# Kernel tuning notes

Measured on AMD Instinct MI355X. Metric: run time of the kernel, lower is better.

The kernel has to match this reference:

```python
import jax, jax.numpy as jnp
import numpy as np

B, N, C = 8, 16384, 256
HEADS = 8
TOK = 4  # token_size = (4, 4)


def _unfold3(x):
    # x: (b, c, h, w) -> (b, c, 9, h, w); 3x3 neighborhood, zero padded.
    b, c, h, w = x.shape
    p = jnp.pad(x, ((0, 0), (0, 0), (1, 1), (1, 1)))
    pat = jnp.stack([p[:, :, 1 + dy:1 + dy + h, 1 + dx:1 + dx + w]
                     for dy in (-1, 0, 1) for dx in (-1, 0, 1)], axis=2)
    return pat


def _fold3(u):
    # u: (b, k, 9, h, w) -> (b, k, h, w); scatter-add inverse of _unfold3
    # (matches F.conv_transpose2d with eye(9) kernels, stride 1, pad 1).
    b, k, _, h, w = u.shape
    p = jnp.pad(u, ((0, 0), (0, 0), (0, 0), (1, 1), (1, 1)))
    out = jnp.zeros((b, k, h, w), u.dtype)
    i = 0
    for dy in (-1, 0, 1):
        for dx in (-1, 0, 1):
            out = out + p[:, :, i, 1 - dy:1 - dy + h, 1 - dx:1 - dx + w]
            i += 1
    return out


def setup_inputs() -> dict:
    key = jax.random.key(0)
    k1, k2, k3, k4 = jax.random.split(key, 4)
    x = jax.random.normal(k1, (B, N, C), jnp.float32)
    qkv_w = jax.random.normal(k2, (3 * C, C), jnp.float32) * 0.02
    proj_w = jax.random.normal(k3, (C, C), jnp.float32) * 0.02
    proj_b = jax.random.normal(k4, (C,), jnp.float32) * 0.02
    return {"x": x, "qkv_w": qkv_w, "proj_w": proj_w, "proj_b": proj_b}


def reference(x, qkv_w, proj_w, proj_b):
    b, n, c = x.shape
    H = W = int(np.sqrt(n))
    hh, ww = H // TOK, W // TOK
    nw = hh * ww                      # number of super tokens
    scale = c ** -0.5
    hd = c // HEADS
    head_scale = hd ** -0.5

    xi = jnp.transpose(x, (0, 2, 1)).reshape(b, c, H, W)
    blocks = xi.reshape(b, c, hh, TOK, ww, TOK)
    wf = blocks.mean(axis=(3, 5))                      # (b,c,hh,ww) adaptive avg pool
    pix = blocks.transpose(0, 2, 4, 3, 5, 1).reshape(b, nw, TOK * TOK, c)

    # 3x3 super-token neighborhood features: (b, nw, c, 9)
    wfu = _unfold3(wf).reshape(b, c, 9, nw).transpose(0, 3, 1, 2)

    # pixel <-> super-token affinity, softmax over 9 neighbors
    aff = jax.nn.softmax(jnp.einsum('bnpc,bnck->bnpk', pix, wfu) * scale, axis=-1)

    # normalization: fold of per-window affinity mass -> (b,1,hh,ww)
    aff_sum = _fold3(aff.sum(2).transpose(0, 2, 1).reshape(b, 1, 9, hh, ww))

    # aggregate pixels into super tokens and fold neighborhoods back
    wf2 = jnp.einsum('bnpc,bnpk->bnck', pix, aff)      # (b,nw,c,9)
    wf2 = _fold3(wf2.transpose(0, 2, 3, 1).reshape(b, c, 9, hh, ww))  # (b,c,hh,ww)
    wf2 = wf2 / (jax.lax.stop_gradient(aff_sum) + 1e-12)

    # inner attention over super tokens (non-SDPA: softmax over key axis)
    qkv = jnp.einsum('oc,bchw->bohw', qkv_w, wf2).reshape(b, HEADS, 3 * hd, nw)
    q, k, v = jnp.split(qkv, 3, axis=2)                # each (b,heads,hd,nw)
    attn = jnp.einsum('bhdn,bhdm->bhnm', k, q) * head_scale
    attn = jax.nn.softmax(attn, axis=-2)               # softmax over key index n
    ref = jnp.einsum('bhdn,bhnm->bhdm', v, attn).reshape(b, c, hh, ww)
    ref = jnp.einsum('oc,bchw->bohw', proj_w, ref) + proj_b[None, :, None, None]

    # scatter refined super tokens back to pixels through the affinity
    wfu2 = _unfold3(ref).reshape(b, c, 9, nw).transpose(0, 3, 1, 2)   # (b,nw,c,9)
    pix2 = jnp.einsum('bnck,bnpk->bncp', wfu2, aff)    # (b,nw,c,16)
    pix2 = pix2.reshape(b, hh, ww, c, TOK, TOK).transpose(0, 3, 1, 4, 2, 5)
    pix2 = pix2.reshape(b, c, H, W)
    # NOTE: torch does a raw memory reshape (B,C,H,W)->(B,H*W,C), not a transpose;
    # we replicate that exactly.
    return pix2.reshape(b, H * W, c)
```

## Files before the change

### kernel.cpp

```cpp
#include <hip/hip_runtime.h>

typedef short short8 __attribute__((ext_vector_type(8)));
typedef float f32x4 __attribute__((ext_vector_type(4)));

__device__ __forceinline__ unsigned short f2bf(float x) {
  union { float f; unsigned int u; } v; v.f = x;
  unsigned int r = (v.u + 0x7FFFu + ((v.u >> 16) & 1u)) >> 16;
  return (unsigned short)r;
}

__global__ __launch_bounds__(256) void k0_wconv(const float* __restrict__ qkvw,
                                                const float* __restrict__ projw,
                                                unsigned short* __restrict__ wqkvbf,
                                                unsigned short* __restrict__ wprojbf) {
  int i = blockIdx.x * 256 + threadIdx.x;
  if (i < 768 * 256) wqkvbf[i] = f2bf(qkvw[i]);
  if (i < 256 * 256) wprojbf[i] = f2bf(projw[i]);
}

__global__ __launch_bounds__(256) void k1_pool(const float* __restrict__ x,
                                               float* __restrict__ wf) {
  int t = threadIdx.x;
  int blk = blockIdx.x;
  int b = blk >> 10, pos = blk & 1023;
  int y = pos >> 5, xw = pos & 31;
  const float* xb = x + (size_t)b * 4194304;
  float acc = 0.f;
  #pragma unroll
  for (int p = 0; p < 16; ++p) {
    int h = 4 * y + (p >> 2), w = 4 * xw + (p & 3);
    acc += xb[(size_t)(h * 128 + w) * 256 + t];
  }
  wf[(size_t)blk * 256 + t] = acc * 0.0625f;
}

__global__ __launch_bounds__(256) void k2_winaff(const float* __restrict__ x,
                                                 const float* __restrict__ wf,
                                                 float* __restrict__ aff_g,
                                                 float* __restrict__ wf2acc,
                                                 float* __restrict__ asumacc) {
  __shared__ float pixs[16][257];
  __shared__ float wfu[9][257];
  __shared__ float aff_s[16][12];
  int t = threadIdx.x;
  int blk = blockIdx.x;
  int b = blk >> 10, pos = blk & 1023;
  int y = pos >> 5, xw = pos & 31;
  const float* xb = x + (size_t)b * 4194304;

  #pragma unroll
  for (int p = 0; p < 16; ++p) {
    int h = 4 * y + (p >> 2), w = 4 * xw + (p & 3);
    pixs[p][t] = xb[(size_t)(h * 128 + w) * 256 + t];
  }
  #pragma unroll
  for (int i = 0; i < 9; ++i) {
    int dy = i / 3 - 1, dx = i % 3 - 1;
    int ny = y + dy, nx = xw + dx;
    float v = 0.f;
    if (ny >= 0 && ny < 32 && nx >= 0 && nx < 32)
      v = wf[((size_t)(b * 1024) + ny * 32 + nx) * 256 + t];
    wfu[i][t] = v;
  }
  __syncthreads();

  if (t < 144) {
    int p = t / 9, i = t - p * 9;
    float acc = 0.f;
    #pragma unroll 8
    for (int c = 0; c < 256; ++c) acc += pixs[p][c] * wfu[i][c];
    aff_s[p][i] = acc * 0.0625f;
  }
  __syncthreads();

  if (t < 16) {
    float m = aff_s[t][0];
    #pragma unroll
    for (int i = 1; i < 9; ++i) m = fmaxf(m, aff_s[t][i]);
    float e[9]; float s = 0.f;
    #pragma unroll
    for (int i = 0; i < 9; ++i) { e[i] = __expf(aff_s[t][i] - m); s += e[i]; }
    float inv = 1.f / s;
    #pragma unroll
    for (int i = 0; i < 9; ++i) aff_s[t][i] = e[i] * inv;
  }
  __syncthreads();

  if (t < 144) aff_g[(size_t)blk * 144 + t] = aff_s[t / 9][t % 9];

  if (t < 9) {
    int dy = t / 3 - 1, dx = t % 3 - 1;
    int ny = y + dy, nx = xw + dx;
    if (ny >= 0 && ny < 32 && nx >= 0 && nx < 32) {
      float s = 0.f;
      #pragma unroll
      for (int p = 0; p < 16; ++p) s += aff_s[p][t];
      atomicAdd(&asumacc[b * 1024 + ny * 32 + nx], s);
    }
  }

  #pragma unroll
  for (int i = 0; i < 9; ++i) {
    int dy = i / 3 - 1, dx = i % 3 - 1;
    int ny = y + dy, nx = xw + dx;
    if (ny < 0 || ny >= 32 || nx < 0 || nx >= 32) continue;
    float acc = 0.f;
    #pragma unroll
    for (int p = 0; p < 16; ++p) acc += pixs[p][t] * aff_s[p][i];
    atomicAdd(&wf2acc[((size_t)(b * 1024) + ny * 32 + nx) * 256 + t], acc);
  }
}

__global__ __launch_bounds__(256) void k3_norm(const float* __restrict__ wf2acc,
                                               const float* __restrict__ asumacc,
                                               unsigned short* __restrict__ wf2bf) {
  int t = threadIdx.x;
  for (int u = blockIdx.x; u < 8192; u += 2048) {
    float den = asumacc[u] + 1e-12f;
    float v = wf2acc[(size_t)u * 256 + t] / den;
    wf2bf[(size_t)u * 256 + t] = f2bf(v);
  }
}

__global__ __launch_bounds__(256) void k4_qkv(const unsigned short* __restrict__ wbf,
                                              const unsigned short* __restrict__ xbf,
                                              unsigned short* __restrict__ qt,
                                              unsigned short* __restrict__ kt,
                                              unsigned short* __restrict__ vt) {
  int tid = threadIdx.x, lane = tid & 63, wv = tid >> 6;
  int l15 = lane & 15, g = lane >> 4;
  int nb = blockIdx.x * 64 + (wv & 1) * 32;
  int ob = blockIdx.y * 64 + (wv >> 1) * 32;
  int b = blockIdx.z;
  const unsigned short* X = xbf + (size_t)b * 262144;
  f32x4 acc[2][2] = {};
  for (int cc = 0; cc < 256; cc += 32) {
    short8 af[2], bfr[2];
    #pragma unroll
    for (int oi = 0; oi < 2; ++oi)
      af[oi] = *(const short8*)(wbf + (size_t)(ob + oi * 16 + l15) * 256 + cc + g * 8);
    #pragma unroll
    for (int ni = 0; ni < 2; ++ni)
      bfr[ni] = *(const short8*)(X + (size_t)(nb + ni * 16 + l15) * 256 + cc + g * 8);
    #pragma unroll
    for (int oi = 0; oi < 2; ++oi)
      #pragma unroll
      for (int ni = 0; ni < 2; ++ni)
        acc[oi][ni] = __builtin_amdgcn_mfma_f32_16x16x32_bf16(af[oi], bfr[ni], acc[oi][ni], 0, 0, 0);
  }
  #pragma unroll
  for (int oi = 0; oi < 2; ++oi)
    #pragma unroll
    for (int ni = 0; ni < 2; ++ni)
      #pragma unroll
      for (int r = 0; r < 4; ++r) {
        int o = ob + oi * 16 + g * 4 + r;
        int n = nb + ni * 16 + l15;
        unsigned short bv = f2bf(acc[oi][ni][r]);
        int head = o / 96;
        int rr = o - head * 96;
        size_t bh = (size_t)(b * 8 + head);
        if (rr < 32) qt[(bh * 1024 + n) * 32 + rr] = bv;
        else if (rr < 64) kt[(bh * 1024 + n) * 32 + (rr - 32)] = bv;
        else vt[(bh * 32 + (rr - 64)) * 1024 + n] = bv;
      }
}

__global__ __launch_bounds__(256) void k5_attn(const unsigned short* __restrict__ qt,
                                               const unsigned short* __restrict__ kt,
                                               const unsigned short* __restrict__ vt,
                                               unsigned short* __restrict__ refpre) {
  __shared__ short P_lds[4][32][40];
  __shared__ float out_lds[4][32][33];
  __shared__ float den_lds[4][32];
  int tid = threadIdx.x, lane = tid & 63, wv = tid >> 6;
  int l15 = lane & 15, g = lane >> 4;
  int mt = blockIdx.x, h = blockIdx.y, b = blockIdx.z;
  const unsigned short* qtb = qt + ((size_t)(b * 8 + h) * 1024) * 32;
  const unsigned short* ktb = kt + ((size_t)(b * 8 + h) * 1024) * 32;
  const unsigned short* vtb = vt + ((size_t)(b * 8 + h) * 32) * 1024;

  short8 qf[2];
  #pragma unroll
  for (int mi = 0; mi < 2; ++mi) {
    int m = mt * 32 + mi * 16 + l15;
    qf[mi] = *(const short8*)(qtb + (size_t)m * 32 + g * 8);
  }
  f32x4 oacc[2][2] = {};
  float dsum0 = 0.f, dsum1 = 0.f;
  const float hs = 0.17677669529663687f;

  for (int c8 = 0; c8 < 8; ++c8) {
    int nchunk = wv * 256 + c8 * 32;
    f32x4 sf[2][2];
    #pragma unroll
    for (int nt = 0; nt < 2; ++nt) {
      int n = nchunk + nt * 16 + l15;
      short8 kf = *(const short8*)(ktb + (size_t)n * 32 + g * 8);
      #pragma unroll
      for (int mi = 0; mi < 2; ++mi) {
        f32x4 z = {0.f, 0.f, 0.f, 0.f};
        sf[nt][mi] = __builtin_amdgcn_mfma_f32_16x16x32_bf16(kf, qf[mi], z, 0, 0, 0);
      }
    }
    #pragma unroll
    for (int nt = 0; nt < 2; ++nt)
      #pragma unroll
      for (int mi = 0; mi < 2; ++mi) {
        float p0 = __expf(hs * sf[nt][mi][0]);
        float p1 = __expf(hs * sf[nt][mi][1]);
        float p2 = __expf(hs * sf[nt][mi][2]);
        float p3 = __expf(hs * sf[nt][mi][3]);
        float ds = (p0 + p1) + (p2 + p3);
        if (mi == 0) dsum0 += ds; else dsum1 += ds;
        unsigned int w01 = ((unsigned int)f2bf(p1) << 16) | f2bf(p0);
        unsigned int w23 = ((unsigned int)f2bf(p3) << 16) | f2bf(p2);
        int ml = mi * 16 + l15;
        int nn = nt * 16 + g * 4;
        *(unsigned int*)&P_lds[wv][ml][nn] = w01;
        *(unsigned int*)&P_lds[wv][ml][nn + 2] = w23;
      }
    #pragma unroll
    for (int dh = 0; dh < 2; ++dh) {
      short8 vf = *(const short8*)(vtb + (size_t)(dh * 16 + l15) * 1024 + nchunk + g * 8);
      #pragma unroll
      for (int mi = 0; mi < 2; ++mi) {
        short8 pf = *(const short8*)&P_lds[wv][mi * 16 + l15][g * 8];
        oacc[dh][mi] = __builtin_amdgcn_mfma_f32_16x16x32_bf16(vf, pf, oacc[dh][mi], 0, 0, 0);
      }
    }
  }

  dsum0 += __shfl_xor(dsum0, 16); dsum0 += __shfl_xor(dsum0, 32);
  dsum1 += __shfl_xor(dsum1, 16); dsum1 += __shfl_xor(dsum1, 32);
  if (lane < 16) { den_lds[wv][lane] = dsum0; den_lds[wv][16 + lane] = dsum1; }
  #pragma unroll
  for (int dh = 0; dh < 2; ++dh)
    #pragma unroll
    for (int mi = 0; mi < 2; ++mi)
      #pragma unroll
      for (int r = 0; r < 4; ++r)
        out_lds[wv][dh * 16 + g * 4 + r][mi * 16 + l15] = oacc[dh][mi][r];
  __syncthreads();

  #pragma unroll
  for (int kk = 0; kk < 4; ++kk) {
    int idx = kk * 256 + tid;
    int d = idx & 31, m = idx >> 5;
    float v = out_lds[0][d][m] + out_lds[1][d][m] + out_lds[2][d][m] + out_lds[3][d][m];
    float den = den_lds[0][m] + den_lds[1][m] + den_lds[2][m] + den_lds[3][m];
    float res = v / den;
    int n = mt * 32 + m;
    refpre[((size_t)(b * 1024) + n) * 256 + h * 32 + d] = f2bf(res);
  }
}

__global__ __launch_bounds__(256) void k6_proj(const unsigned short* __restrict__ wbf,
                                               const unsigned short* __restrict__ xbf,
                                               const float* __restrict__ bias,
                                               float* __restrict__ reft) {
  int tid = threadIdx.x, lane = tid & 63, wv = tid >> 6;
  int l15 = lane & 15, g = lane >> 4;
  int nb = blockIdx.x * 64 + (wv & 1) * 32;
  int ob = blockIdx.y * 64 + (wv >> 1) * 32;
  int b = blockIdx.z;
  const unsigned short* X = xbf + (size_t)b * 262144;
  f32x4 acc[2][2] = {};
  for (int cc = 0; cc < 256; cc += 32) {
    short8 af[2], bfr[2];
    #pragma unroll
    for (int oi = 0; oi < 2; ++oi)
      af[oi] = *(const short8*)(wbf + (size_t)(ob + oi * 16 + l15) * 256 + cc + g * 8);
    #pragma unroll
    for (int ni = 0; ni < 2; ++ni)
      bfr[ni] = *(const short8*)(X + (size_t)(nb + ni * 16 + l15) * 256 + cc + g * 8);
    #pragma unroll
    for (int oi = 0; oi < 2; ++oi)
      #pragma unroll
      for (int ni = 0; ni < 2; ++ni)
        acc[oi][ni] = __builtin_amdgcn_mfma_f32_16x16x32_bf16(af[oi], bfr[ni], acc[oi][ni], 0, 0, 0);
  }
  #pragma unroll
  for (int oi = 0; oi < 2; ++oi)
    #pragma unroll
    for (int ni = 0; ni < 2; ++ni) {
      int o4 = ob + oi * 16 + g * 4;
      int n = nb + ni * 16 + l15;
      f32x4 b4 = *(const f32x4*)(bias + o4);
      f32x4 r = acc[oi][ni] + b4;
      *(f32x4*)(reft + ((size_t)(b * 1024) + n) * 256 + o4) = r;
    }
}

__global__ __launch_bounds__(256) void k7_scatter(const float* __restrict__ reft,
                                                  const float* __restrict__ aff_g,
                                                  float* __restrict__ out) {
  __shared__ float refn[32 * 3 * 34];
  __shared__ float affl[144 * 33];
  int t = threadIdx.x;
  int cg = blockIdx.x;
  int y = blockIdx.y;
  int b = blockIdx.z;
  int c0 = cg * 32;

  for (int i = t; i < 32 * 3 * 34; i += 256) {
    int c = i & 31;
    int rest = i >> 5;
    int xx = rest % 34;
    int dy = rest / 34;
    int ny = y + dy - 1, nx = xx - 1;
    float v = 0.f;
    if (ny >= 0 && ny < 32 && nx >= 0 && nx < 32)
      v = reft[((size_t)(b * 1024) + ny * 32 + nx) * 256 + c0 + c];
    refn[(c * 3 + dy) * 34 + xx] = v;
  }
  for (int i = t; i < 4608; i += 256) {
    int xw = i / 144;
    int rem = i - xw * 144;
    affl[rem * 33 + xw] = aff_g[((size_t)(b * 1024) + y * 32) * 144 + i];
  }
  __syncthreads();

  for (int kk = 0; kk < 64; ++kk) {
    int idx = kk * 256 + t;
    int wpix = idx & 127;
    int rest = idx >> 7;
    int ii = rest & 3, c = rest >> 2;
    int xw = wpix >> 2, j = wpix & 3;
    int p = ii * 4 + j;
    float acc = 0.f;
    #pragma unroll
    for (int k = 0; k < 9; ++k) {
      int dy = k / 3, kx = k % 3;
      acc += refn[(c * 3 + dy) * 34 + xw + kx] * affl[(p * 9 + k) * 33 + xw];
    }
    out[(size_t)b * 4194304 + (size_t)(c0 + c) * 16384 + (4 * y + ii) * 128 + wpix] = acc;
  }
}

extern "C" void kernel_launch(void* const* d_in, const int* in_sizes, int n_in,
                              void* d_out, int out_size, void* d_ws, size_t ws_size,
                              hipStream_t stream) {
  const float* x = (const float*)d_in[0];
  const float* qkvw = (const float*)d_in[1];
  const float* projw = (const float*)d_in[2];
  const float* projb = (const float*)d_in[3];
  float* out = (float*)d_out;
  char* ws = (char*)d_ws;

  float* wf            = (float*)(ws + 0);
  float* wf2acc        = (float*)(ws + 8388608);
  float* asumacc       = (float*)(ws + 16777216);
  float* aff           = (float*)(ws + 16809984);
  unsigned short* wf2bf  = (unsigned short*)(ws + 21528576);
  unsigned short* qt     = (unsigned short*)(ws + 25722880);
  unsigned short* kt     = (unsigned short*)(ws + 29917184);
  unsigned short* vt     = (unsigned short*)(ws + 34111488);
  unsigned short* refpre = (unsigned short*)(ws + 38305792);
  float* reft          = (float*)(ws + 42500096);
  unsigned short* wqkvbf = (unsigned short*)(ws + 50888704);
  unsigned short* wprojbf= (unsigned short*)(ws + 51281920);

  hipMemsetAsync(wf2acc, 0, 8388608 + 32768, stream);
  k0_wconv<<<768, 256, 0, stream>>>(qkvw, projw, wqkvbf, wprojbf);
  k1_pool<<<8192, 256, 0, stream>>>(x, wf);
  k2_winaff<<<8192, 256, 0, stream>>>(x, wf, aff, wf2acc, asumacc);
  k3_norm<<<2048, 256, 0, stream>>>(wf2acc, asumacc, wf2bf);
  k4_qkv<<<dim3(16, 12, 8), 256, 0, stream>>>(wqkvbf, wf2bf, qt, kt, vt);
  k5_attn<<<dim3(32, 8, 8), 256, 0, stream>>>(qt, kt, vt, refpre);
  k6_proj<<<dim3(16, 4, 8), 256, 0, stream>>>(wprojbf, refpre, projb, reft);
  k7_scatter<<<dim3(8, 32, 8), 256, 0, stream>>>(reft, aff, out);
}
```

Measured before the change: 412.2 us.

## Replace atomic fold scatter with per-window bf16 partials and gather kernel

The window-affinity kernel now writes each window's 9 neighbor contributions as bf16 partials plus per-neighbor affinity sums, instead of issuing float atomicAdds into a shared accumulator. A new gather kernel sums the 9 contributions per super token and normalizes, so the memset and the atomic contention go away. The affinity dot products are also spread across all 256 threads with shuffle reductions, where before only 144 threads looped serially over channels. In exchange it writes and reads a roughly 37 MB bf16 intermediate and rounds the partial sums to bf16 before accumulation.

```diff
diff --git a/kernel.cpp b/kernel.cpp
--- a/kernel.cpp
+++ b/kernel.cpp
@@ -7,6 +7,10 @@
   union { float f; unsigned int u; } v; v.f = x;
   unsigned int r = (v.u + 0x7FFFu + ((v.u >> 16) & 1u)) >> 16;
   return (unsigned short)r;
+}
+__device__ __forceinline__ float bf2f(unsigned short u) {
+  union { unsigned int u; float f; } v; v.u = ((unsigned int)u) << 16;
+  return v.f;
 }
 
 __global__ __launch_bounds__(256) void k0_wconv(const float* __restrict__ qkvw,
@@ -37,10 +41,10 @@
 __global__ __launch_bounds__(256) void k2_winaff(const float* __restrict__ x,
                                                  const float* __restrict__ wf,
                                                  float* __restrict__ aff_g,
-                                                 float* __restrict__ wf2acc,
-                                                 float* __restrict__ asumacc) {
-  __shared__ float pixs[16][257];
-  __shared__ float wfu[9][257];
+                                                 unsigned short* __restrict__ agg,
+                                                 float* __restrict__ asum_w) {
+  __shared__ float pixs[16][272];
+  __shared__ float wfu[9][272];
   __shared__ float aff_s[16][12];
   int t = threadIdx.x;
   int blk = blockIdx.x;
@@ -64,12 +68,17 @@
   }
   __syncthreads();
 
-  if (t < 144) {
-    int p = t / 9, i = t - p * 9;
+  int pp = t >> 4, sub = t & 15;
+  #pragma unroll
+  for (int i = 0; i < 9; ++i) {
     float acc = 0.f;
-    #pragma unroll 8
-    for (int c = 0; c < 256; ++c) acc += pixs[p][c] * wfu[i][c];
-    aff_s[p][i] = acc * 0.0625f;
+    #pragma unroll
+    for (int j = 0; j < 16; ++j) acc += pixs[pp][sub + 16 * j] * wfu[i][sub + 16 * j];
+    acc += __shfl_xor(acc, 1);
+    acc += __shfl_xor(acc, 2);
+    acc += __shfl_xor(acc, 4);
+    acc += __shfl_xor(acc, 8);
+    if (sub == 0) aff_s[pp][i] = acc * 0.0625f;
   }
   __syncthreads();
 
@@ -87,39 +96,40 @@
   __syncthreads();
 
   if (t < 144) aff_g[(size_t)blk * 144 + t] = aff_s[t / 9][t % 9];
-
   if (t < 9) {
-    int dy = t / 3 - 1, dx = t % 3 - 1;
-    int ny = y + dy, nx = xw + dx;
-    if (ny >= 0 && ny < 32 && nx >= 0 && nx < 32) {
-      float s = 0.f;
-      #pragma unroll
-      for (int p = 0; p < 16; ++p) s += aff_s[p][t];
-      atomicAdd(&asumacc[b * 1024 + ny * 32 + nx], s);
-    }
-  }
-
+    float s = 0.f;
+    #pragma unroll
+    for (int p = 0; p < 16; ++p) s += aff_s[p][t];
+    asum_w[blk * 9 + t] = s;
+  }
+
+  #pragma unroll
+  for (int k = 0; k < 9; ++k) {
+    float acc = 0.f;
+    #pragma unroll
+    for (int p = 0; p < 16; ++p) acc += pixs[p][t] * aff_s[p][k];
+    agg[((size_t)blk * 9 + k) * 256 + t] = f2bf(acc);
+  }
+}
+
+__global__ __launch_bounds__(256) void k3_gather(const unsigned short* __restrict__ agg,
+                                                 const float* __restrict__ asum_w,
+                                                 unsigned short* __restrict__ wf2bf) {
+  int t = threadIdx.x;
+  int blk = blockIdx.x;
+  int b = blk >> 10, pos = blk & 1023;
+  int y = pos >> 5, xw = pos & 31;
+  float acc = 0.f, den = 0.f;
   #pragma unroll
   for (int i = 0; i < 9; ++i) {
     int dy = i / 3 - 1, dx = i % 3 - 1;
-    int ny = y + dy, nx = xw + dx;
-    if (ny < 0 || ny >= 32 || nx < 0 || nx >= 32) continue;
-    float acc = 0.f;
-    #pragma unroll
-    for (int p = 0; p < 16; ++p) acc += pixs[p][t] * aff_s[p][i];
-    atomicAdd(&wf2acc[((size_t)(b * 1024) + ny * 32 + nx) * 256 + t], acc);
-  }
-}
-
-__global__ __launch_bounds__(256) void k3_norm(const float* __restrict__ wf2acc,
-                                               const float* __restrict__ asumacc,
-                                               unsigned short* __restrict__ wf2bf) {
-  int t = threadIdx.x;
-  for (int u = blockIdx.x; u < 8192; u += 2048) {
-    float den = asumacc[u] + 1e-12f;
-    float v = wf2acc[(size_t)u * 256 + t] / den;
-    wf2bf[(size_t)u * 256 + t] = f2bf(v);
-  }
+    int sy = y - dy, sx = xw - dx;
+    if (sy < 0 || sy >= 32 || sx < 0 || sx >= 32) continue;
+    size_t un = (size_t)(b * 1024) + sy * 32 + sx;
+    acc += bf2f(agg[(un * 9 + i) * 256 + t]);
+    den += asum_w[un * 9 + i];
+  }
+  wf2bf[(size_t)blk * 256 + t] = f2bf(acc / (den + 1e-12f));
 }
 
 __global__ __launch_bounds__(256) void k4_qkv(const unsigned short* __restrict__ wbf,
@@ -348,24 +358,23 @@
   float* out = (float*)d_out;
   char* ws = (char*)d_ws;
 
-  float* wf            = (float*)(ws + 0);
-  float* wf2acc        = (float*)(ws + 8388608);
-  float* asumacc       = (float*)(ws + 16777216);
-  float* aff           = (float*)(ws + 16809984);
-  unsigned short* wf2bf  = (unsigned short*)(ws + 21528576);
-  unsigned short* qt     = (unsigned short*)(ws + 25722880);
-  unsigned short* kt     = (unsigned short*)(ws + 29917184);
-  unsigned short* vt     = (unsigned short*)(ws + 34111488);
-  unsigned short* refpre = (unsigned short*)(ws + 38305792);
-  float* reft          = (float*)(ws + 42500096);
-  unsigned short* wqkvbf = (unsigned short*)(ws + 50888704);
-  unsigned short* wprojbf= (unsigned short*)(ws + 51281920);
-
-  hipMemsetAsync(wf2acc, 0, 8388608 + 32768, stream);
+  float* wf             = (float*)(ws + 0);
+  float* aff            = (float*)(ws + 8388608);
+  unsigned short* agg   = (unsigned short*)(ws + 13107200);
+  float* asum_w         = (float*)(ws + 50855936);
+  unsigned short* wf2bf = (unsigned short*)(ws + 51150848);
+  unsigned short* qt    = (unsigned short*)(ws + 55345152);
+  unsigned short* kt    = (unsigned short*)(ws + 59539456);
+  unsigned short* vt    = (unsigned short*)(ws + 63733760);
+  unsigned short* refpre= (unsigned short*)(ws + 67928064);
+  float* reft           = (float*)(ws + 72122368);
+  unsigned short* wqkvbf = (unsigned short*)(ws + 80510976);
+  unsigned short* wprojbf= (unsigned short*)(ws + 80904192);
+
   k0_wconv<<<768, 256, 0, stream>>>(qkvw, projw, wqkvbf, wprojbf);
   k1_pool<<<8192, 256, 0, stream>>>(x, wf);
-  k2_winaff<<<8192, 256, 0, stream>>>(x, wf, aff, wf2acc, asumacc);
-  k3_norm<<<2048, 256, 0, stream>>>(wf2acc, asumacc, wf2bf);
+  k2_winaff<<<8192, 256, 0, stream>>>(x, wf, aff, agg, asum_w);
+  k3_gather<<<8192, 256, 0, stream>>>(agg, asum_w, wf2bf);
   k4_qkv<<<dim3(16, 12, 8), 256, 0, stream>>>(wqkvbf, wf2bf, qt, kt, vt);
   k5_attn<<<dim3(32, 8, 8), 256, 0, stream>>>(qt, kt, vt, refpre);
   k6_proj<<<dim3(16, 4, 8), 256, 0, stream>>>(wprojbf, refpre, projb, reft);
```

Result: no change. 414.6 us (+0.6%).
